# Kernel tuning notes

Measured on AMD Instinct MI355X. Metric: run time of the kernel, lower is better.

Reference implementation:

```python
import jax, jax.numpy as jnp
import numpy as np

MAX_DEPTH = 9
HIDDEN = 64
EMB = 64
POS_FREQS = 6
IN_C = 1
SIZES = [4 ** d for d in range(MAX_DEPTH + 1)]
OFFSETS = np.concatenate([[0], np.cumsum(SIZES)])  # per-depth slices into concatenated node arrays
TOTAL = int(OFFSETS[-1])  # 349525
POS_DIM = 3 + 2 * POS_FREQS * 3  # 39


def _interleave(v):
    v = v & 0xFFFF
    v = (v | (v << 8)) & 0x00FF00FF
    v = (v | (v << 4)) & 0x0F0F0F0F
    v = (v | (v << 2)) & 0x33333333
    v = (v | (v << 1)) & 0x55555555
    return v


def _deinterleave(v):
    v = v & 0x55555555
    v = (v | (v >> 1)) & 0x33333333
    v = (v | (v >> 2)) & 0x0F0F0F0F
    v = (v | (v >> 4)) & 0x00FF00FF
    v = (v | (v >> 8)) & 0x0000FFFF
    return v


def _xy(d):
    keys = jnp.arange(4 ** d, dtype=jnp.int32)  # full tree: sorted Morton keys = arange
    return _deinterleave(keys), _deinterleave(keys >> 1)


def _neighbors(d):
    # [N, 9] neighbor indices in Morton order grid; -1 outside the image (matches quadtree.neighs padding)
    ix, iy = _xy(d)
    res = 1 << d
    cols = []
    for dy in (-1, 0, 1):
        for dx in (-1, 0, 1):
            nx, ny = ix + dx, iy + dy
            valid = (nx >= 0) & (nx < res) & (ny >= 0) & (ny < res)
            key = _interleave(nx) | (_interleave(ny) << 1)
            cols.append(jnp.where(valid, key, -1))
    return jnp.stack(cols, axis=1)


def _pos_enc(d):
    # node_centers_from_keys + fourier_encode
    ix, iy = _xy(d)
    res = float(1 << d)
    x = (ix.astype(jnp.float32) + 0.5) / res
    y = (iy.astype(jnp.float32) + 0.5) / res
    dn = jnp.full_like(x, float(d) / float(MAX_DEPTH))
    pos = jnp.stack([x, y, dn], axis=1)  # [N, 3]
    freqs = 2.0 ** jnp.arange(POS_FREQS, dtype=jnp.float32)
    ang = pos[:, :, None] * (2.0 * np.pi) * freqs  # [N, 3, F]
    enc = jnp.concatenate([jnp.sin(ang), jnp.cos(ang)], axis=-1).reshape(pos.shape[0], -1)  # [N, 3*2F]
    return jnp.concatenate([pos, enc], axis=1)  # [N, 39]


def setup_inputs() -> dict:
    key = jax.random.key(0)
    ks = jax.random.split(key, 10)
    s = 0.05
    return {
        "features_in": jax.random.normal(ks[0], (TOTAL, IN_C), jnp.float32),
        "in_proj_W": jax.random.normal(ks[1], (IN_C + POS_DIM, HIDDEN), jnp.float32) * s,
        "in_proj_b": jnp.zeros((HIDDEN,), jnp.float32),
        "conv_W": jax.random.normal(ks[2], (MAX_DEPTH + 1, 9 * HIDDEN, HIDDEN), jnp.float32) * s,
        "conv_b": jnp.zeros((MAX_DEPTH + 1, HIDDEN), jnp.float32),
        "emb_W": jax.random.normal(ks[3], (MAX_DEPTH + 1, HIDDEN, EMB), jnp.float32) * s,
        "emb_b": jnp.zeros((MAX_DEPTH + 1, EMB), jnp.float32),
        "ln_g": jnp.ones((MAX_DEPTH + 1, EMB), jnp.float32),
        "ln_b": jnp.zeros((MAX_DEPTH + 1, EMB), jnp.float32),
        "depth_gain": jnp.ones((MAX_DEPTH + 1,), jnp.float32),
    }


def reference(features_in, in_proj_W, in_proj_b, conv_W, conv_b, emb_W, emb_b, ln_g, ln_b, depth_gain):
    D = MAX_DEPTH
    # per-depth input projection with fourier positional encoding
    h = []
    for d in range(D + 1):
        f = features_in[OFFSETS[d]:OFFSETS[d + 1]]
        x = jnp.concatenate([f, _pos_enc(d)], axis=1)  # [N_d, in_c + 39]
        h.append(x @ in_proj_W + in_proj_b)
    # bottom-up: QuadPool (mean over 4 children; full tree => children of parent i are 4i..4i+3) + QuadConv
    for d in range(D, 0, -1):
        Np = 4 ** (d - 1)
        pooled = h[d].reshape(Np, 4, HIDDEN).mean(axis=1)
        hd1 = h[d - 1] + pooled
        if d - 1 >= 1:
            neigh = _neighbors(d - 1)  # [N, 9], -1 at borders
            N = neigh.shape[0]
            padded = jnp.concatenate([hd1, jnp.zeros((1, HIDDEN), hd1.dtype)], axis=0)
            gi = jnp.where(neigh < 0, N, neigh)
            col = padded[gi].reshape(N, 9 * HIDDEN)
            hd1 = jax.nn.relu(col @ conv_W[d - 1] + conv_b[d - 1])
        h[d - 1] = hd1
    # per-depth embedding head: Linear -> LayerNorm -> depth gain
    outs = []
    eps = 1e-5
    for d in range(D + 1):
        z = h[d] @ emb_W[d] + emb_b[d]
        mu = z.mean(-1, keepdims=True)
        var = ((z - mu) ** 2).mean(-1, keepdims=True)
        z = (z - mu) / jnp.sqrt(var + eps) * ln_g[d] + ln_b[d]
        outs.append(depth_gain[d] * z)
    return jnp.concatenate(outs, axis=0)  # [TOTAL, EMB] (E[0]..E[max_depth] concatenated)
```

## Files before the change

kernel.cpp:

```cpp
#include <hip/hip_runtime.h>
#include <hip/hip_bf16.h>

static constexpr int TOTAL = 349525;
static constexpr int OFFS[11] = {0,1,5,21,85,341,1365,5461,21845,87381,349525};
static constexpr int EB64[11] = {0,1,2,3,4,8,24,88,344,1368,5464};
static constexpr size_t CONV_USH = (size_t)8*9*2*4*64*8;
static constexpr size_t EMB_USH  = (size_t)10*2*4*64*8;
static constexpr size_t FRAG_USH = CONV_USH + EMB_USH;
static constexpr size_t FRAG_BYTES = FRAG_USH*2*2;
static constexpr size_t HPRE_BYTES = (size_t)(87381-85)*64*4;

typedef __attribute__((ext_vector_type(8))) short short8;
typedef __attribute__((ext_vector_type(4))) float f32x4;

__device__ __forceinline__ unsigned deint(unsigned v){
  v &= 0x55555555u;
  v = (v | (v>>1)) & 0x33333333u;
  v = (v | (v>>2)) & 0x0F0F0F0Fu;
  v = (v | (v>>4)) & 0x00FF00FFu;
  v = (v | (v>>8)) & 0x0000FFFFu;
  return v;
}
__device__ __forceinline__ unsigned ileave(unsigned v){
  v &= 0xFFFFu;
  v = (v | (v<<8)) & 0x00FF00FFu;
  v = (v | (v<<4)) & 0x0F0F0F0Fu;
  v = (v | (v<<2)) & 0x33333333u;
  v = (v | (v<<1)) & 0x55555555u;
  return v;
}
__device__ __forceinline__ unsigned short f2bh(float x){
  unsigned u = __float_as_uint(x);
  return (unsigned short)((u + 0x7FFFu + ((u>>16)&1u)) >> 16);
}
__device__ __forceinline__ float bh2f(unsigned short h){
  return __uint_as_float(((unsigned)h) << 16);
}
__device__ __forceinline__ void split8(float4 a, float4 b, short8 &hi, short8 &lo){
  float v[8] = {a.x,a.y,a.z,a.w,b.x,b.y,b.z,b.w};
  unsigned short hv[8], lv[8];
  #pragma unroll
  for (int j=0;j<8;++j){ hv[j]=f2bh(v[j]); lv[j]=f2bh(v[j]-bh2f(hv[j])); }
  hi = short8{(short)hv[0],(short)hv[1],(short)hv[2],(short)hv[3],
              (short)hv[4],(short)hv[5],(short)hv[6],(short)hv[7]};
  lo = short8{(short)lv[0],(short)lv[1],(short)lv[2],(short)lv[3],
              (short)lv[4],(short)lv[5],(short)lv[6],(short)lv[7]};
}

__global__ __launch_bounds__(256) void k_wprep(const float* __restrict__ convW,
    const float* __restrict__ embW,
    unsigned short* __restrict__ WH, unsigned short* __restrict__ WLo){
  int tid = blockIdx.x*256 + threadIdx.x;
  if (tid >= 41984) return;
  const float* src;
  size_t dst;
  if (tid < 36864){
    int l=tid&63, cb=(tid>>6)&3, ks=(tid>>8)&1;
    int x=tid>>9; int m=x%9, Lp=x/9;
    int k0=ks*32+((l>>4)<<3), ch=cb*16+(l&15);
    src = convW + (size_t)(Lp+1)*36864 + (size_t)(m*64+k0)*64 + ch;
    dst = (size_t)tid*8;
  } else {
    int t2 = tid - 36864;
    int l=t2&63, cb=(t2>>6)&3, ks=(t2>>8)&1, d=t2>>9;
    int k0=ks*32+((l>>4)<<3), ch=cb*16+(l&15);
    src = embW + (size_t)d*4096 + (size_t)k0*64 + ch;
    dst = CONV_USH + (size_t)t2*8;
  }
  unsigned short hv[8], lv[8];
  #pragma unroll
  for (int j=0;j<8;++j){
    float v = src[(size_t)j*64];
    unsigned short h = f2bh(v);
    hv[j] = h;
    lv[j] = f2bh(v - bh2f(h));
  }
  short8 vh = {(short)hv[0],(short)hv[1],(short)hv[2],(short)hv[3],
               (short)hv[4],(short)hv[5],(short)hv[6],(short)hv[7]};
  short8 vl = {(short)lv[0],(short)lv[1],(short)lv[2],(short)lv[3],
               (short)lv[4],(short)lv[5],(short)lv[6],(short)lv[7]};
  *(short8*)(WH  + dst) = vh;
  *(short8*)(WLo + dst) = vl;
}

__global__ __launch_bounds__(256) void k_inproj(const float* __restrict__ feat,
    const float* __restrict__ W, const float* __restrict__ B,
    float* __restrict__ h, float* __restrict__ hpre){
  __shared__ float Alt[128][44];
  __shared__ float Wl[40][68];
  int t = threadIdx.x;
  int base = blockIdx.x * 128;
  for (int idx = t; idx < 40*64; idx += 256)
    Wl[idx >> 6][idx & 63] = W[idx];
  if (t < 128){
    int g = base + t;
    float* row = Alt[t];
    if (g < TOTAL){
      int d = 0;
      #pragma unroll
      for (int i = 1; i <= 9; ++i) if (g >= OFFS[i]) d = i;
      int local = g - OFFS[d];
      unsigned ix = deint((unsigned)local), iy = deint(((unsigned)local) >> 1);
      float inv = 1.0f / (float)(1 << d);
      float px = ((float)ix + 0.5f) * inv;
      float py = ((float)iy + 0.5f) * inv;
      float pd = (float)d * (1.0f/9.0f);
      row[0] = feat[g]; row[1] = px; row[2] = py; row[3] = pd;
      float p3[3] = {px, py, pd};
      #pragma unroll
      for (int c = 0; c < 3; ++c){
        float s, co;
        __sincosf(6.28318530717958647692f * p3[c], &s, &co);
        float* rb = row + 4 + c*12;
        #pragma unroll
        for (int f = 0; f < 6; ++f){
          rb[f] = s; rb[6+f] = co;
          float s2 = 2.f*s*co, c2 = 1.f - 2.f*s*s;
          s = s2; co = c2;
        }
      }
    } else {
      #pragma unroll
      for (int k = 0; k < 40; ++k) row[k] = 0.f;
    }
  }
  __syncthreads();
  int tr = t >> 3, tc = t & 7;
  float acc[4][8];
  #pragma unroll
  for (int i=0;i<4;++i)
    #pragma unroll
    for (int c=0;c<8;++c) acc[i][c] = 0.f;
  #pragma unroll 2
  for (int k4 = 0; k4 < 10; ++k4){
    float av4[4][4];
    #pragma unroll
    for (int i=0;i<4;++i){
      float4 aa = *(const float4*)&Alt[tr*4+i][k4*4];
      av4[i][0]=aa.x; av4[i][1]=aa.y; av4[i][2]=aa.z; av4[i][3]=aa.w;
    }
    #pragma unroll
    for (int j=0;j<4;++j){
      float4 lo = *(const float4*)&Wl[k4*4+j][tc*8];
      float4 hi = *(const float4*)&Wl[k4*4+j][tc*8+4];
      float wv[8];
      wv[0]=lo.x; wv[1]=lo.y; wv[2]=lo.z; wv[3]=lo.w;
      wv[4]=hi.x; wv[5]=hi.y; wv[6]=hi.z; wv[7]=hi.w;
      #pragma unroll
      for (int i=0;i<4;++i){
        float a = av4[i][j];
        #pragma unroll
        for (int c=0;c<8;++c) acc[i][c] += a*wv[c];
      }
    }
  }
  #pragma unroll
  for (int i=0;i<4;++i){
    int g = base + tr*4 + i;
    if (g >= TOTAL) continue;
    float ov[8];
    #pragma unroll
    for (int c=0;c<8;++c) ov[c] = acc[i][c] + B[tc*8+c];
    float* dst = &h[(size_t)g*64 + tc*8];
    *(float4*)dst       = *(const float4*)&ov[0];
    *(float4*)(dst + 4) = *(const float4*)&ov[4];
    if (hpre && g >= OFFS[4] && g < OFFS[9]){
      float* dp = hpre + (size_t)(g - OFFS[4])*64 + tc*8;
      *(float4*)dp       = *(const float4*)&ov[0];
      *(float4*)(dp + 4) = *(const float4*)&ov[4];
    }
  }
}

__global__ __launch_bounds__(256) void k_conv(float* __restrict__ h,
    const float* __restrict__ hPar,
    const unsigned short* __restrict__ WHl, const unsigned short* __restrict__ WLl,
    const float* __restrict__ Bb, int N, int offL, int offC, int lbits){
  __shared__ unsigned short haloH[100*72];
  __shared__ unsigned short haloL[100*72];
  __shared__ int hkey[100];
  int t = threadIdx.x;
  int nb = blockIdx.x * 64;
  int res = 1 << lbits;
  if (t < 100){
    int i = t % 10, j = t / 10;
    int gx = (int)deint((unsigned)nb) - 1 + i;
    int gy = (int)deint(((unsigned)nb)>>1) - 1 + j;
    bool ok = (gx>=0 && gy>=0 && gx<res && gy<res);
    hkey[t] = ok ? (int)(ileave((unsigned)gx) | (ileave((unsigned)gy)<<1)) : -1;
  }
  __syncthreads();
  const float* hC = h + (size_t)offC*64;
  for (int e = t; e < 1600; e += 256){
    int hi_ = e >> 4, u = e & 15;
    int key = hkey[hi_];
    float4 r = make_float4(0.f,0.f,0.f,0.f);
    if (key >= 0){
      const float4* c = (const float4*)(hC + (size_t)(4*key)*64) + u;
      float4 c0 = c[0], c1 = c[16], c2 = c[32], c3 = c[48];
      float4 pr = *((const float4*)(hPar + (size_t)key*64) + u);
      r.x = 0.25f*(c0.x+c1.x+c2.x+c3.x) + pr.x;
      r.y = 0.25f*(c0.y+c1.y+c2.y+c3.y) + pr.y;
      r.z = 0.25f*(c0.z+c1.z+c2.z+c3.z) + pr.z;
      r.w = 0.25f*(c0.w+c1.w+c2.w+c3.w) + pr.w;
    }
    unsigned short h0=f2bh(r.x), h1=f2bh(r.y), h2=f2bh(r.z), h3=f2bh(r.w);
    ushort4 rh = make_ushort4(h0,h1,h2,h3);
    ushort4 rl = make_ushort4(f2bh(r.x - bh2f(h0)), f2bh(r.y - bh2f(h1)),
                              f2bh(r.z - bh2f(h2)), f2bh(r.w - bh2f(h3)));
    *(ushort4*)&haloH[hi_*72 + u*4] = rh;
    *(ushort4*)&haloL[hi_*72 + u*4] = rl;
  }
  __syncthreads();

  int cb   = __builtin_amdgcn_readfirstlane((int)(threadIdx.x >> 6));
  int lane = t & 63;
  int q = lane >> 4;
  int chl = cb*16 + (lane & 15);
  int lx0,ly0,lx1,ly1,lx2,ly2,lx3,ly3;
  {
    int n0 = (lane&15), n1 = 16+(lane&15), n2 = 32+(lane&15), n3 = 48+(lane&15);
    lx0=(int)deint((unsigned)n0); ly0=(int)deint(((unsigned)n0)>>1);
    lx1=(int)deint((unsigned)n1); ly1=(int)deint(((unsigned)n1)>>1);
    lx2=(int)deint((unsigned)n2); ly2=(int)deint(((unsigned)n2)>>1);
    lx3=(int)deint((unsigned)n3); ly3=(int)deint(((unsigned)n3)>>1);
  }
  f32x4 acc0 = {0.f,0.f,0.f,0.f}, acc1 = acc0, acc2 = acc0, acc3 = acc0;

  #pragma unroll 1
  for (int dy=0;dy<3;++dy){
    #pragma unroll 1
    for (int dx=0;dx<3;++dx){
      int m = dy*3 + dx;
      int r0 = (ly0+dy)*10 + lx0+dx;
      int r1 = (ly1+dy)*10 + lx1+dx;
      int r2 = (ly2+dy)*10 + lx2+dx;
      int r3 = (ly3+dy)*10 + lx3+dx;
      #pragma unroll
      for (int ks=0;ks<2;++ks){
        const unsigned short* fp = WHl + ((size_t)((m*2+ks)*4 + cb)*64 + lane)*8;
        const unsigned short* fq = WLl + ((size_t)((m*2+ks)*4 + cb)*64 + lane)*8;
        short8 bh = *(const short8*)fp;
        short8 bl = *(const short8*)fq;
        int so = (ks*4 + q)*8;
        short8 ah0 = *(const short8*)&haloH[r0*72 + so];
        short8 al0 = *(const short8*)&haloL[r0*72 + so];
        short8 ah1 = *(const short8*)&haloH[r1*72 + so];
        short8 al1 = *(const short8*)&haloL[r1*72 + so];
        short8 ah2 = *(const short8*)&haloH[r2*72 + so];
        short8 al2 = *(const short8*)&haloL[r2*72 + so];
        short8 ah3 = *(const short8*)&haloH[r3*72 + so];
        short8 al3 = *(const short8*)&haloL[r3*72 + so];
        acc0 = __builtin_amdgcn_mfma_f32_16x16x32_bf16(ah0, bh, acc0, 0,0,0);
        acc1 = __builtin_amdgcn_mfma_f32_16x16x32_bf16(ah1, bh, acc1, 0,0,0);
        acc2 = __builtin_amdgcn_mfma_f32_16x16x32_bf16(ah2, bh, acc2, 0,0,0);
        acc3 = __builtin_amdgcn_mfma_f32_16x16x32_bf16(ah3, bh, acc3, 0,0,0);
        acc0 = __builtin_amdgcn_mfma_f32_16x16x32_bf16(al0, bh, acc0, 0,0,0);
        acc1 = __builtin_amdgcn_mfma_f32_16x16x32_bf16(al1, bh, acc1, 0,0,0);
        acc2 = __builtin_amdgcn_mfma_f32_16x16x32_bf16(al2, bh, acc2, 0,0,0);
        acc3 = __builtin_amdgcn_mfma_f32_16x16x32_bf16(al3, bh, acc3, 0,0,0);
        acc0 = __builtin_amdgcn_mfma_f32_16x16x32_bf16(ah0, bl, acc0, 0,0,0);
        acc1 = __builtin_amdgcn_mfma_f32_16x16x32_bf16(ah1, bl, acc1, 0,0,0);
        acc2 = __builtin_amdgcn_mfma_f32_16x16x32_bf16(ah2, bl, acc2, 0,0,0);
        acc3 = __builtin_amdgcn_mfma_f32_16x16x32_bf16(ah3, bl, acc3, 0,0,0);
      }
    }
  }
  float bias = Bb[chl];
  int rowb = q*4;
  float* hO = h + (size_t)(offL + nb)*64;
  #pragma unroll
  for (int reg=0;reg<4;++reg){
    int n0 = rowb + reg;
    float v0 = acc0[reg] + bias; if (nb + n0      < N) hO[(size_t)(n0     )*64 + chl] = v0 > 0.f ? v0 : 0.f;
    float v1 = acc1[reg] + bias; if (nb + n0 + 16 < N) hO[(size_t)(n0 + 16)*64 + chl] = v1 > 0.f ? v1 : 0.f;
    float v2 = acc2[reg] + bias; if (nb + n0 + 32 < N) hO[(size_t)(n0 + 32)*64 + chl] = v2 > 0.f ? v2 : 0.f;
    float v3 = acc3[reg] + bias; if (nb + n0 + 48 < N) hO[(size_t)(n0 + 48)*64 + chl] = v3 > 0.f ? v3 : 0.f;
  }
}

template<int L>
__device__ __forceinline__ void tail_level(float* __restrict__ h,
    const unsigned short* __restrict__ WHc, const unsigned short* __restrict__ WLc,
    const float* __restrict__ convB,
    unsigned short* __restrict__ PtH, unsigned short* __restrict__ PtL, int t){
  constexpr int Np  = 1 << (2*L);
  constexpr int NTt = (Np + 15)/16;
  constexpr int TG  = (NTt + 3)/4;
  constexpr int res = 1 << L;
  for (int e = t; e < (Np+1)*16; e += 1024){
    int node = e >> 4, u = e & 15;
    float4 r = make_float4(0.f,0.f,0.f,0.f);
    if (node < Np){
      const float4* c = (const float4*)(h + (size_t)(OFFS[L+1] + 4*node)*64) + u;
      float4 c0 = c[0], c1 = c[16], c2 = c[32], c3 = c[48];
      float4 pr = *((const float4*)(h + (size_t)(OFFS[L] + node)*64) + u);
      r.x = 0.25f*(c0.x+c1.x+c2.x+c3.x) + pr.x;
      r.y = 0.25f*(c0.y+c1.y+c2.y+c3.y) + pr.y;
      r.z = 0.25f*(c0.z+c1.z+c2.z+c3.z) + pr.z;
      r.w = 0.25f*(c0.w+c1.w+c2.w+c3.w) + pr.w;
    }
    unsigned short h0=f2bh(r.x), h1=f2bh(r.y), h2=f2bh(r.z), h3=f2bh(r.w);
    *(ushort4*)&PtH[node*72 + u*4] = make_ushort4(h0,h1,h2,h3);
    *(ushort4*)&PtL[node*72 + u*4] = make_ushort4(
        f2bh(r.x - bh2f(h0)), f2bh(r.y - bh2f(h1)),
        f2bh(r.z - bh2f(h2)), f2bh(r.w - bh2f(h3)));
  }
  __syncthreads();
  int w  = t >> 6;
  int cb = __builtin_amdgcn_readfirstlane(w & 3);
  int tg = __builtin_amdgcn_readfirstlane(w >> 2);
  int lane = t & 63;
  int q = lane >> 4;
  int chl = cb*16 + (lane & 15);
  int lx[TG], ly[TG];
  #pragma unroll
  for (int i=0;i<TG;++i){
    unsigned n = (unsigned)((tg*TG + i)*16 + (lane & 15));
    lx[i] = (int)deint(n); ly[i] = (int)deint(n >> 1);
  }
  f32x4 acc[TG];
  #pragma unroll
  for (int i=0;i<TG;++i) acc[i] = f32x4{0.f,0.f,0.f,0.f};
  #pragma unroll 1
  for (int m=0;m<9;++m){
    int dy = m/3 - 1, dx = m%3 - 1;
    size_t f0 = ((size_t)((m*2+0)*4 + cb)*64 + lane)*8;
    size_t f1 = ((size_t)((m*2+1)*4 + cb)*64 + lane)*8;
    short8 bh0 = *(const short8*)(WHc + f0);
    short8 bl0 = *(const short8*)(WLc + f0);
    short8 bh1 = *(const short8*)(WHc + f1);
    short8 bl1 = *(const short8*)(WLc + f1);
    #pragma unroll
    for (int i=0;i<TG;++i){
      int nx = lx[i]+dx, ny = ly[i]+dy;
      int key = (nx>=0 && ny>=0 && nx<res && ny<res)
              ? (int)(ileave((unsigned)nx) | (ileave((unsigned)ny)<<1)) : Np;
      const unsigned short* pH = PtH + key*72;
      const unsigned short* pL = PtL + key*72;
      short8 ah0 = *(const short8*)(pH + q*8);
      short8 al0 = *(const short8*)(pL + q*8);
      short8 ah1 = *(const short8*)(pH + 32 + q*8);
      short8 al1 = *(const short8*)(pL + 32 + q*8);
      acc[i] = __builtin_amdgcn_mfma_f32_16x16x32_bf16(ah0, bh0, acc[i], 0,0,0);
      acc[i] = __builtin_amdgcn_mfma_f32_16x16x32_bf16(al0, bh0, acc[i], 0,0,0);
      acc[i] = __builtin_amdgcn_mfma_f32_16x16x32_bf16(ah0, bl0, acc[i], 0,0,0);
      acc[i] = __builtin_amdgcn_mfma_f32_16x16x32_bf16(ah1, bh1, acc[i], 0,0,0);
      acc[i] = __builtin_amdgcn_mfma_f32_16x16x32_bf16(al1, bh1, acc[i], 0,0,0);
      acc[i] = __builtin_amdgcn_mfma_f32_16x16x32_bf16(ah1, bl1, acc[i], 0,0,0);
    }
  }
  float bias = convB[L*64 + chl];
  #pragma unroll
  for (int i=0;i<TG;++i){
    #pragma unroll
    for (int reg=0;reg<4;++reg){
      int ni = (tg*TG + i)*16 + q*4 + reg;
      if (ni < Np){
        float v = acc[i][reg] + bias;
        h[(size_t)(OFFS[L] + ni)*64 + chl] = v > 0.f ? v : 0.f;
      }
    }
  }
  __syncthreads();
}

__global__ __launch_bounds__(1024) void k_tail(float* __restrict__ h,
    const unsigned short* __restrict__ WH, const unsigned short* __restrict__ WLo,
    const float* __restrict__ convB){
  __shared__ unsigned short PtH[257*72];
  __shared__ unsigned short PtL[257*72];
  int t = threadIdx.x;
  tail_level<4>(h, WH + (size_t)3*36864, WLo + (size_t)3*36864, convB, PtH, PtL, t);
  tail_level<3>(h, WH + (size_t)2*36864, WLo + (size_t)2*36864, convB, PtH, PtL, t);
  tail_level<2>(h, WH + (size_t)1*36864, WLo + (size_t)1*36864, convB, PtH, PtL, t);
  tail_level<1>(h, WH,                   WLo,                   convB, PtH, PtL, t);
  if (t < 16){
    const float4* c = (const float4*)(h + (size_t)OFFS[1]*64) + t;
    float4 c0 = c[0], c1 = c[16], c2 = c[32], c3 = c[48];
    float4 pr = ((const float4*)h)[t];
    float4 r;
    r.x = 0.25f*(c0.x+c1.x+c2.x+c3.x) + pr.x;
    r.y = 0.25f*(c0.y+c1.y+c2.y+c3.y) + pr.y;
    r.z = 0.25f*(c0.z+c1.z+c2.z+c3.z) + pr.z;
    r.w = 0.25f*(c0.w+c1.w+c2.w+c3.w) + pr.w;
    ((float4*)h)[t] = r;
  }
}

__global__ __launch_bounds__(256) void k_emb(float* __restrict__ h,
    const unsigned short* __restrict__ EH, const unsigned short* __restrict__ ELo,
    const float* __restrict__ embB, const float* __restrict__ lng,
    const float* __restrict__ lnb, const float* __restrict__ gain){
  int bb = blockIdx.x;
  int d = 0;
  #pragma unroll
  for (int i=1;i<=9;++i) if (bb >= EB64[i]) d = i;
  int nb = (bb - EB64[d]) * 64;
  int N = 1 << (2*d);
  int off = OFFS[d];
  int t = threadIdx.x;
  int wt = __builtin_amdgcn_readfirstlane(t >> 6);
  int lane = t & 63;
  int q = lane >> 4, li = lane & 15;

  const float* rp = h + ((size_t)off + nb + wt*16 + li)*64 + q*8;
  float4 a0 = *(const float4*)rp;
  float4 a1 = *(const float4*)(rp + 4);
  float4 a2 = *(const float4*)(rp + 32);
  float4 a3 = *(const float4*)(rp + 36);
  short8 ah0, al0, ah1, al1;
  split8(a0, a1, ah0, al0);
  split8(a2, a3, ah1, al1);

  f32x4 acc0 = {0.f,0.f,0.f,0.f}, acc1 = acc0, acc2 = acc0, acc3 = acc0;
  #define EMB_CB(CB, ACC) { \
    size_t f0 = (((size_t)(d*2+0)*4 + (CB))*64 + lane)*8; \
    size_t f1 = (((size_t)(d*2+1)*4 + (CB))*64 + lane)*8; \
    short8 bh0 = *(const short8*)(EH + f0); \
    short8 bl0 = *(const short8*)(ELo + f0); \
    short8 bh1 = *(const short8*)(EH + f1); \
    short8 bl1 = *(const short8*)(ELo + f1); \
    ACC = __builtin_amdgcn_mfma_f32_16x16x32_bf16(ah0, bh0, ACC, 0,0,0); \
    ACC = __builtin_amdgcn_mfma_f32_16x16x32_bf16(al0, bh0, ACC, 0,0,0); \
    ACC = __builtin_amdgcn_mfma_f32_16x16x32_bf16(ah0, bl0, ACC, 0,0,0); \
    ACC = __builtin_amdgcn_mfma_f32_16x16x32_bf16(ah1, bh1, ACC, 0,0,0); \
    ACC = __builtin_amdgcn_mfma_f32_16x16x32_bf16(al1, bh1, ACC, 0,0,0); \
    ACC = __builtin_amdgcn_mfma_f32_16x16x32_bf16(ah1, bl1, ACC, 0,0,0); }
  EMB_CB(0, acc0)
  EMB_CB(1, acc1)
  EMB_CB(2, acc2)
  EMB_CB(3, acc3)
  #undef EMB_CB

  float b0 = embB[d*64 +      li];
  float b1 = embB[d*64 + 16 + li];
  float b2 = embB[d*64 + 32 + li];
  float b3 = embB[d*64 + 48 + li];
  float mu[4], rs[4];
  float z0[4], z1[4], z2[4], z3[4];
  #pragma unroll
  for (int r=0;r<4;++r){
    z0[r] = acc0[r] + b0;
    z1[r] = acc1[r] + b1;
    z2[r] = acc2[r] + b2;
    z3[r] = acc3[r] + b3;
    float s  = z0[r] + z1[r] + z2[r] + z3[r];
    float qv = z0[r]*z0[r] + z1[r]*z1[r] + z2[r]*z2[r] + z3[r]*z3[r];
    #pragma unroll
    for (int mk=1; mk<16; mk<<=1){
      s  += __shfl_xor(s, mk, 64);
      qv += __shfl_xor(qv, mk, 64);
    }
    float m = s * 0.015625f;
    mu[r] = m;
    rs[r] = rsqrtf(qv * 0.015625f - m*m + 1e-5f);
  }
  float g0 = lng[d*64 +      li], l0 = lnb[d*64 +      li];
  float g1 = lng[d*64 + 16 + li], l1 = lnb[d*64 + 16 + li];
  float g2 = lng[d*64 + 32 + li], l2 = lnb[d*64 + 32 + li];
  float g3 = lng[d*64 + 48 + li], l3 = lnb[d*64 + 48 + li];
  float gn = gain[d];
  #pragma unroll
  for (int r=0;r<4;++r){
    int ni = wt*16 + q*4 + r;
    if (nb + ni < N){
      float* row = h + ((size_t)off + nb + ni)*64;
      row[     li] = ((z0[r] - mu[r])*rs[r]*g0 + l0)*gn;
      row[16 + li] = ((z1[r] - mu[r])*rs[r]*g1 + l1)*gn;
      row[32 + li] = ((z2[r] - mu[r])*rs[r]*g2 + l2)*gn;
      row[48 + li] = ((z3[r] - mu[r])*rs[r]*g3 + l3)*gn;
    }
  }
}

extern "C" void kernel_launch(void* const* d_in, const int* in_sizes, int n_in,
                              void* d_out, int out_size, void* d_ws, size_t ws_size,
                              hipStream_t stream) {
  (void)in_sizes; (void)n_in; (void)out_size;
  const float* feat  = (const float*)d_in[0];
  const float* ipW   = (const float*)d_in[1];
  const float* ipB   = (const float*)d_in[2];
  const float* convW = (const float*)d_in[3];
  const float* convB = (const float*)d_in[4];
  const float* embW  = (const float*)d_in[5];
  const float* embB  = (const float*)d_in[6];
  const float* lng   = (const float*)d_in[7];
  const float* lnb   = (const float*)d_in[8];
  const float* gain  = (const float*)d_in[9];
  float* h = (float*)d_out;

  unsigned short* WH  = (unsigned short*)d_ws;
  unsigned short* WLo = WH + FRAG_USH;
  float* hpre = (ws_size >= FRAG_BYTES + HPRE_BYTES)
              ? (float*)((char*)d_ws + FRAG_BYTES) : nullptr;

  k_wprep<<<164, 256, 0, stream>>>(convW, embW, WH, WLo);
  k_inproj<<<(TOTAL + 127)/128, 256, 0, stream>>>(feat, ipW, ipB, h, hpre);

  for (int L = 8; L >= 5; --L){
    int Np = 1 << (2*L);
    const float* hPar = hpre ? (hpre + (size_t)(OFFS[L] - OFFS[4])*64)
                             : (h + (size_t)OFFS[L]*64);
    k_conv<<<Np/64, 256, 0, stream>>>(h, hPar,
        WH  + (size_t)(L-1)*36864, WLo + (size_t)(L-1)*36864,
        convB + (size_t)L*64, Np, OFFS[L], OFFS[L+1], L);
  }

  k_tail<<<1, 1024, 0, stream>>>(h, WH, WLo, convB);
  k_emb<<<5464, 256, 0, stream>>>(h, WH + CONV_USH, WLo + CONV_USH,
                                  embB, lng, lnb, gain);
}
```

Measured before the change: 219.3 us.

## Fuse tail-level pooling into conv epilogue via registers and LDS-cached parents

The single-block tail kernel now computes each level's pooled parent input straight from the conv accumulators held in registers. It writes that result as bf16 hi/lo into LDS, so the next level no longer re-reads the just-written children from global memory. Parent rows for depths 0-3 are cached in LDS once at kernel start. Weight fragments for the next neighbor tap are prefetched one iteration ahead. This removes a global round trip and a sync stage per level, at the cost of extra LDS use and registers.

```diff
diff --git a/kernel.cpp b/kernel.cpp
--- a/kernel.cpp
+++ b/kernel.cpp
@@ -280,57 +280,46 @@
 }
 
 template<int L>
-__device__ __forceinline__ void tail_level(float* __restrict__ h,
+__device__ __forceinline__ void tail_level2(float* __restrict__ h,
     const unsigned short* __restrict__ WHc, const unsigned short* __restrict__ WLc,
-    const float* __restrict__ convB,
+    const float* __restrict__ convB, const float* __restrict__ Hpar,
     unsigned short* __restrict__ PtH, unsigned short* __restrict__ PtL, int t){
   constexpr int Np  = 1 << (2*L);
   constexpr int NTt = (Np + 15)/16;
   constexpr int TG  = (NTt + 3)/4;
   constexpr int res = 1 << L;
-  for (int e = t; e < (Np+1)*16; e += 1024){
-    int node = e >> 4, u = e & 15;
-    float4 r = make_float4(0.f,0.f,0.f,0.f);
-    if (node < Np){
-      const float4* c = (const float4*)(h + (size_t)(OFFS[L+1] + 4*node)*64) + u;
-      float4 c0 = c[0], c1 = c[16], c2 = c[32], c3 = c[48];
-      float4 pr = *((const float4*)(h + (size_t)(OFFS[L] + node)*64) + u);
-      r.x = 0.25f*(c0.x+c1.x+c2.x+c3.x) + pr.x;
-      r.y = 0.25f*(c0.y+c1.y+c2.y+c3.y) + pr.y;
-      r.z = 0.25f*(c0.z+c1.z+c2.z+c3.z) + pr.z;
-      r.w = 0.25f*(c0.w+c1.w+c2.w+c3.w) + pr.w;
-    }
-    unsigned short h0=f2bh(r.x), h1=f2bh(r.y), h2=f2bh(r.z), h3=f2bh(r.w);
-    *(ushort4*)&PtH[node*72 + u*4] = make_ushort4(h0,h1,h2,h3);
-    *(ushort4*)&PtL[node*72 + u*4] = make_ushort4(
-        f2bh(r.x - bh2f(h0)), f2bh(r.y - bh2f(h1)),
-        f2bh(r.z - bh2f(h2)), f2bh(r.w - bh2f(h3)));
-  }
-  __syncthreads();
   int w  = t >> 6;
   int cb = __builtin_amdgcn_readfirstlane(w & 3);
   int tg = __builtin_amdgcn_readfirstlane(w >> 2);
   int lane = t & 63;
-  int q = lane >> 4;
-  int chl = cb*16 + (lane & 15);
+  int q = lane >> 4, li = lane & 15;
+  int chl = cb*16 + li;
   int lx[TG], ly[TG];
   #pragma unroll
   for (int i=0;i<TG;++i){
-    unsigned n = (unsigned)((tg*TG + i)*16 + (lane & 15));
+    unsigned n = (unsigned)((tg*TG + i)*16 + li);
     lx[i] = (int)deint(n); ly[i] = (int)deint(n >> 1);
   }
   f32x4 acc[TG];
   #pragma unroll
   for (int i=0;i<TG;++i) acc[i] = f32x4{0.f,0.f,0.f,0.f};
+  short8 bh0, bl0, bh1, bl1;
+  {
+    size_t f0 = ((size_t)(0*4 + cb)*64 + lane)*8;
+    size_t f1 = ((size_t)(1*4 + cb)*64 + lane)*8;
+    bh0 = *(const short8*)(WHc + f0); bl0 = *(const short8*)(WLc + f0);
+    bh1 = *(const short8*)(WHc + f1); bl1 = *(const short8*)(WLc + f1);
+  }
   #pragma unroll 1
   for (int m=0;m<9;++m){
+    short8 nh0, nl0, nh1, nl1;
+    if (m < 8){
+      size_t f0 = ((size_t)(((m+1)*2+0)*4 + cb)*64 + lane)*8;
+      size_t f1 = ((size_t)(((m+1)*2+1)*4 + cb)*64 + lane)*8;
+      nh0 = *(const short8*)(WHc + f0); nl0 = *(const short8*)(WLc + f0);
+      nh1 = *(const short8*)(WHc + f1); nl1 = *(const short8*)(WLc + f1);
+    }
     int dy = m/3 - 1, dx = m%3 - 1;
-    size_t f0 = ((size_t)((m*2+0)*4 + cb)*64 + lane)*8;
-    size_t f1 = ((size_t)((m*2+1)*4 + cb)*64 + lane)*8;
-    short8 bh0 = *(const short8*)(WHc + f0);
-    short8 bl0 = *(const short8*)(WLc + f0);
-    short8 bh1 = *(const short8*)(WHc + f1);
-    short8 bl1 = *(const short8*)(WLc + f1);
     #pragma unroll
     for (int i=0;i<TG;++i){
       int nx = lx[i]+dx, ny = ly[i]+dy;
@@ -349,17 +338,40 @@
       acc[i] = __builtin_amdgcn_mfma_f32_16x16x32_bf16(al1, bh1, acc[i], 0,0,0);
       acc[i] = __builtin_amdgcn_mfma_f32_16x16x32_bf16(ah1, bl1, acc[i], 0,0,0);
     }
+    if (m < 8){ bh0 = nh0; bl0 = nl0; bh1 = nh1; bl1 = nl1; }
   }
   float bias = convB[L*64 + chl];
+  float vq[TG][4];
   #pragma unroll
   for (int i=0;i<TG;++i){
     #pragma unroll
     for (int reg=0;reg<4;++reg){
       int ni = (tg*TG + i)*16 + q*4 + reg;
-      if (ni < Np){
-        float v = acc[i][reg] + bias;
-        h[(size_t)(OFFS[L] + ni)*64 + chl] = v > 0.f ? v : 0.f;
+      float v = acc[i][reg] + bias;
+      v = v > 0.f ? v : 0.f;
+      vq[i][reg] = v;
+      if (ni < Np) h[(size_t)(OFFS[L] + ni)*64 + chl] = v;
+    }
+  }
+  __syncthreads();
+  if (L > 1){
+    constexpr int Pp = Np/4;
+    #pragma unroll
+    for (int i=0;i<TG;++i){
+      int p = (tg*TG + i)*4 + q;
+      if (p < Pp){
+        float pooled = 0.25f*(vq[i][0]+vq[i][1]+vq[i][2]+vq[i][3])
+                     + Hpar[(size_t)(OFFS[L-1] + p)*64 + chl];
+        unsigned short hh = f2bh(pooled);
+        PtH[p*72 + chl] = hh;
+        PtL[p*72 + chl] = f2bh(pooled - bh2f(hh));
       }
+    }
+    if (t < 64){ PtH[Pp*72 + t] = 0; PtL[Pp*72 + t] = 0; }
+  } else {
+    if (tg == 0 && q == 0){
+      float pooled = 0.25f*(vq[0][0]+vq[0][1]+vq[0][2]+vq[0][3]) + Hpar[chl];
+      h[chl] = pooled;
     }
   }
   __syncthreads();
@@ -370,22 +382,33 @@
     const float* __restrict__ convB){
   __shared__ unsigned short PtH[257*72];
   __shared__ unsigned short PtL[257*72];
+  __shared__ float Hpar[85*64];
   int t = threadIdx.x;
-  tail_level<4>(h, WH + (size_t)3*36864, WLo + (size_t)3*36864, convB, PtH, PtL, t);
-  tail_level<3>(h, WH + (size_t)2*36864, WLo + (size_t)2*36864, convB, PtH, PtL, t);
-  tail_level<2>(h, WH + (size_t)1*36864, WLo + (size_t)1*36864, convB, PtH, PtL, t);
-  tail_level<1>(h, WH,                   WLo,                   convB, PtH, PtL, t);
-  if (t < 16){
-    const float4* c = (const float4*)(h + (size_t)OFFS[1]*64) + t;
-    float4 c0 = c[0], c1 = c[16], c2 = c[32], c3 = c[48];
-    float4 pr = ((const float4*)h)[t];
-    float4 r;
-    r.x = 0.25f*(c0.x+c1.x+c2.x+c3.x) + pr.x;
-    r.y = 0.25f*(c0.y+c1.y+c2.y+c3.y) + pr.y;
-    r.z = 0.25f*(c0.z+c1.z+c2.z+c3.z) + pr.z;
-    r.w = 0.25f*(c0.w+c1.w+c2.w+c3.w) + pr.w;
-    ((float4*)h)[t] = r;
-  }
+  for (int e = t; e < 85*16; e += 1024)
+    ((float4*)Hpar)[e] = ((const float4*)h)[e];
+  for (int e = t; e < 257*16; e += 1024){
+    int node = e >> 4, u = e & 15;
+    float4 r = make_float4(0.f,0.f,0.f,0.f);
+    if (node < 256){
+      const float4* c = (const float4*)(h + (size_t)(OFFS[5] + 4*node)*64) + u;
+      float4 c0 = c[0], c1 = c[16], c2 = c[32], c3 = c[48];
+      float4 pr = *((const float4*)(h + (size_t)(OFFS[4] + node)*64) + u);
+      r.x = 0.25f*(c0.x+c1.x+c2.x+c3.x) + pr.x;
+      r.y = 0.25f*(c0.y+c1.y+c2.y+c3.y) + pr.y;
+      r.z = 0.25f*(c0.z+c1.z+c2.z+c3.z) + pr.z;
+      r.w = 0.25f*(c0.w+c1.w+c2.w+c3.w) + pr.w;
+    }
+    unsigned short h0=f2bh(r.x), h1=f2bh(r.y), h2=f2bh(r.z), h3=f2bh(r.w);
+    *(ushort4*)&PtH[node*72 + u*4] = make_ushort4(h0,h1,h2,h3);
+    *(ushort4*)&PtL[node*72 + u*4] = make_ushort4(
+        f2bh(r.x - bh2f(h0)), f2bh(r.y - bh2f(h1)),
+        f2bh(r.z - bh2f(h2)), f2bh(r.w - bh2f(h3)));
+  }
+  __syncthreads();
+  tail_level2<4>(h, WH + (size_t)3*36864, WLo + (size_t)3*36864, convB, Hpar, PtH, PtL, t);
+  tail_level2<3>(h, WH + (size_t)2*36864, WLo + (size_t)2*36864, convB, Hpar, PtH, PtL, t);
+  tail_level2<2>(h, WH + (size_t)1*36864, WLo + (size_t)1*36864, convB, Hpar, PtH, PtL, t);
+  tail_level2<1>(h, WH,                   WLo,                   convB, Hpar, PtH, PtL, t);
 }
 
 __global__ __launch_bounds__(256) void k_emb(float* __restrict__ h,
```

Measured after the change: 205.6 us. -6.3%, faster.
